# Performance work log

Hardware: AMD Instinct MI355X
Metric: run time of the kernel (lower is better)

The kernel has to match this reference:

```python
import jax, jax.numpy as jnp
import numpy as np

T = 2048            # flattened tokens (vLLM style)
D = 4096            # hidden_size
NSSM = 128          # ssm_state_size
K = 4               # conv kernel size
G = 8               # n_groups
H = 128             # mamba_num_heads
P = 64              # mamba_head_dim
INTER = H * P       # 8192 = expand * hidden_size
CONV_DIM = INTER + 2 * G * NSSM   # 10240 (x, B, C share the conv)
PROJ = INTER + CONV_DIM + H       # 18560 (z, xBC, dt)
Q = 128             # SSD chunk size
EPS = 1e-5


def setup_inputs() -> dict:
    key = jax.random.key(0)
    ks = jax.random.split(key, 9)
    s = 0.02
    return {
        "hidden_states": jax.random.normal(ks[0], (T, D), jnp.float32),
        "residual": jax.random.normal(ks[1], (T, D), jnp.float32),
        "norm_w": jnp.ones((D,), jnp.float32),
        "in_proj_w": jax.random.normal(ks[2], (PROJ, D), jnp.float32) * s,
        "conv_w": jax.random.normal(ks[3], (CONV_DIM, K), jnp.float32) * 0.2,
        "conv_b": jax.random.normal(ks[4], (CONV_DIM,), jnp.float32) * 0.1,
        "A_log": jnp.log(jax.random.uniform(ks[5], (H,), jnp.float32, 1.0, 16.0)),
        "D_res": jax.random.normal(ks[6], (H,), jnp.float32) * 0.5 + 1.0,
        "dt_bias": jax.random.normal(ks[7], (H,), jnp.float32) * 0.5,
        "gn_w": jnp.ones((INTER,), jnp.float32),
        "out_proj_w": jax.random.normal(ks[8], (D, INTER), jnp.float32) * s,
    }


def _forward(hidden_states, residual, norm_w, in_proj_w, conv_w, conv_b,
             A_log, D_res, dt_bias, gn_w, out_proj_w):
    # ---- fused add + RMSNorm (vLLM RMSNorm(hidden, residual)) ----
    resid = hidden_states + residual
    hs = resid * jax.lax.rsqrt(jnp.mean(resid * resid, -1, keepdims=True) + EPS) * norm_w

    # ---- MambaMixer2 ----
    proj = hs @ in_proj_w.T                              # [T, PROJ]
    z, xBC, dt = jnp.split(proj, [INTER, INTER + CONV_DIM], axis=-1)

    # causal depthwise conv1d over time + SiLU
    xp = jnp.pad(xBC, ((K - 1, 0), (0, 0)))
    conv = conv_b + sum(conv_w[:, k] * xp[k:k + T] for k in range(K))
    xBC = jax.nn.silu(conv)

    x, B, C = jnp.split(xBC, [INTER, INTER + G * NSSM], axis=-1)
    x = x.reshape(T, H, P)
    Bh = jnp.repeat(B.reshape(T, G, NSSM), H // G, axis=1)   # [T,H,N]
    Ch = jnp.repeat(C.reshape(T, G, NSSM), H // G, axis=1)   # [T,H,N]

    dt = jax.nn.softplus(dt + dt_bias)                   # [T,H]
    A = -jnp.exp(A_log)                                  # [H] (negative)

    # ---- SSD chunked selective scan ----
    NC = T // Q
    a = (dt * A).reshape(NC, Q, H)                       # per-step log decay (<=0)
    cum = jnp.cumsum(a, axis=1)                          # inclusive cumsum, [NC,Q,H]
    Xd = (dt[:, :, None] * x).reshape(NC, Q, H, P)
    Bc = Bh.reshape(NC, Q, H, NSSM)
    Cc = Ch.reshape(NC, Q, H, NSSM)

    # intra-chunk: Y[i] = sum_{j<=i} (C_i.B_j) exp(cum_i-cum_j) Xd_j
    CB = jnp.einsum('cqhn,ckhn->chqk', Cc, Bc)
    cumT = cum.transpose(0, 2, 1)                        # [NC,H,Q]
    mask = jnp.tril(jnp.ones((Q, Q), bool))
    Lm = jnp.where(mask, jnp.exp(cumT[:, :, :, None] - cumT[:, :, None, :]), 0.0)
    Y = jnp.einsum('chqk,ckhp->cqhp', CB * Lm, Xd)

    # chunk-local end states, then scan states across chunks
    cum_end = cum[:, -1]                                 # [NC,H]
    decay_out = jnp.exp(cum_end[:, None] - cum)          # [NC,Q,H]
    S_loc = jnp.einsum('cqhn,cqh,cqhp->chnp', Bc, decay_out, Xd)
    chunk_decay = jnp.exp(cum_end)                       # [NC,H]

    def step(s, inp):
        dec, sl = inp
        return dec[:, None, None] * s + sl, s            # emit state BEFORE chunk

    _, S_prev = jax.lax.scan(step, jnp.zeros((H, NSSM, P), x.dtype),
                             (chunk_decay, S_loc))       # [NC,H,N,P]

    # inter-chunk contribution + skip connection D*x
    Y = Y + jnp.einsum('cqhn,cqh,chnp->cqhp', Cc, jnp.exp(cum), S_prev)
    y = Y.reshape(T, H, P) + D_res[None, :, None] * x

    # gated RMSNorm then out projection
    y = y.reshape(T, INTER) * jax.nn.silu(z)
    y = y * jax.lax.rsqrt(jnp.mean(y * y, -1, keepdims=True) + EPS) * gn_w
    return y @ out_proj_w.T, resid


def reference(hidden_states, residual, norm_w, in_proj_w, conv_w, conv_b,
              A_log, D_res, dt_bias, gn_w, out_proj_w):
    return _forward(hidden_states, residual, norm_w, in_proj_w, conv_w, conv_b,
                    A_log, D_res, dt_bias, gn_w, out_proj_w)
```

## Files before the change

### kernel.cpp

```cpp
#include <hip/hip_runtime.h>
#include <stdint.h>

typedef unsigned short u16;
typedef unsigned int   u32;
typedef float  f32x4  __attribute__((ext_vector_type(4)));
typedef __bf16 bf16x8 __attribute__((ext_vector_type(8)));
typedef u16    u16x4  __attribute__((ext_vector_type(4)));
typedef u16    u16x8  __attribute__((ext_vector_type(8)));

#define T_N     2048
#define D_N     4096
#define H_N     128
#define P_N     64
#define G_N     8
#define NS_N    128
#define INTER_N 8192
#define CONVD_N 10240
#define PROJ_N  18560
#define NGEMM_N 18432
#define NC_N    16

__device__ __forceinline__ float bf2f(u16 u){ u32 x = ((u32)u) << 16; return __builtin_bit_cast(float, x); }
__device__ __forceinline__ u16 f2bf(float f){
  u32 u = __builtin_bit_cast(u32, f);
  u += 0x7FFFu + ((u >> 16) & 1u);
  return (u16)(u >> 16);
}

__device__ __forceinline__ void gld_lds16(const void* g, void* lds){
  __builtin_amdgcn_global_load_lds(
      (const __attribute__((address_space(1))) void*)(uintptr_t)g,
      (__attribute__((address_space(3))) void*)(u32)(uintptr_t)lds,
      16, 0, 0);
}

__global__ __launch_bounds__(256)
void k_addnorm(const float* __restrict__ hin, const float* __restrict__ rin,
               const float* __restrict__ nw, float* __restrict__ resid,
               u16* __restrict__ hs16, float* __restrict__ rstd){
  __shared__ float red[4];
  const int row = blockIdx.x, tid = threadIdx.x;
  const size_t rb = (size_t)row * D_N;
  f32x4 s[4];
  float ss = 0.f;
  #pragma unroll
  for (int i = 0; i < 4; ++i){
    int c4 = tid + i*256;
    f32x4 a = *(const f32x4*)&hin[rb + (size_t)c4*4];
    f32x4 b = *(const f32x4*)&rin[rb + (size_t)c4*4];
    s[i] = a + b;
    *(f32x4*)&resid[rb + (size_t)c4*4] = s[i];
    ss += s[i][0]*s[i][0] + s[i][1]*s[i][1] + s[i][2]*s[i][2] + s[i][3]*s[i][3];
  }
  #pragma unroll
  for (int o = 32; o > 0; o >>= 1) ss += __shfl_down(ss, o, 64);
  if ((tid & 63) == 0) red[tid >> 6] = ss;
  __syncthreads();
  float tot = (red[0] + red[1]) + (red[2] + red[3]);
  float rs = rsqrtf(tot / (float)D_N + 1e-5f);
  if (tid == 0) rstd[row] = rs;
  #pragma unroll
  for (int i = 0; i < 4; ++i){
    int c4 = tid + i*256;
    f32x4 w = *(const f32x4*)&nw[(size_t)c4*4];
    u16x4 o = { f2bf(s[i][0]*rs*w[0]), f2bf(s[i][1]*rs*w[1]),
                f2bf(s[i][2]*rs*w[2]), f2bf(s[i][3]*rs*w[3]) };
    *(u16x4*)&hs16[rb + (size_t)c4*4] = o;
  }
}

__global__ void k_cvt(const float* __restrict__ in, u16* __restrict__ out, size_t n4){
  size_t i = (size_t)blockIdx.x * blockDim.x + threadIdx.x;
  size_t stride = (size_t)gridDim.x * blockDim.x;
  for (; i < n4; i += stride){
    f32x4 v = *(const f32x4*)&in[i*4];
    u16x4 o = { f2bf(v[0]), f2bf(v[1]), f2bf(v[2]), f2bf(v[3]) };
    *(u16x4*)&out[i*4] = o;
  }
}

__global__ void k_wdt(const float* __restrict__ W, const float* __restrict__ nw,
                      float* __restrict__ Wn){
  int idx = blockIdx.x*256 + threadIdx.x;
  int d = idx >> 7, h = idx & 127;
  Wn[(size_t)d*128 + h] = W[(size_t)(INTER_N + CONVD_N + h)*D_N + d] * nw[d];
}

__global__ __launch_bounds__(256)
void k_dtgemm(const float* __restrict__ resid, const float* __restrict__ Wn,
              float* __restrict__ dtpart){
  __shared__ float lhs[16*128];
  const int tid = threadIdx.x;
  const int tb = blockIdx.x >> 3, ks = blockIdx.x & 7;
  const int t0 = tb * 16;
  const int k0 = ks * (D_N / 8);
  const int hcol = tid & 127, rh = tid >> 7;
  float acc[8] = {0,0,0,0,0,0,0,0};
  for (int kt = k0; kt < k0 + D_N/8; kt += 128){
    __syncthreads();
    #pragma unroll
    for (int it = 0; it < 2; ++it){
      int idx = it*256 + tid;
      int rr = idx >> 5, c4 = idx & 31;
      *(f32x4*)&lhs[rr*128 + c4*4] = *(const f32x4*)&resid[(size_t)(t0+rr)*D_N + kt + c4*4];
    }
    __syncthreads();
    #pragma unroll 4
    for (int kk4 = 0; kk4 < 32; ++kk4){
      f32x4 w4;
      #pragma unroll
      for (int j = 0; j < 4; ++j) w4[j] = Wn[(size_t)(kt + kk4*4 + j)*128 + hcol];
      #pragma unroll
      for (int j = 0; j < 8; ++j){
        f32x4 lv = *(const f32x4*)&lhs[(rh*8 + j)*128 + kk4*4];
        acc[j] += lv[0]*w4[0] + lv[1]*w4[1] + lv[2]*w4[2] + lv[3]*w4[3];
      }
    }
  }
  #pragma unroll
  for (int j = 0; j < 8; ++j){
    int t = t0 + rh*8 + j;
    dtpart[((size_t)ks*T_N + t)*128 + hcol] = acc[j];
  }
}

__global__ void k_dtprep(const float* __restrict__ dtpart, const float* __restrict__ rstd,
                         const float* __restrict__ dt_bias, const float* __restrict__ A_log,
                         float* __restrict__ dtv, float* __restrict__ cum,
                         float* __restrict__ cumend, float* __restrict__ dec){
  int c = blockIdx.x, h = threadIdx.x;
  float A = -expf(A_log[h]);
  float bias = dt_bias[h];
  float cm = 0.f;
  for (int q = 0; q < 128; ++q){
    int t = c*128 + q;
    float s = 0.f;
    #pragma unroll
    for (int kspl = 0; kspl < 8; ++kspl)
      s += dtpart[((size_t)kspl*T_N + t)*128 + h];
    float x = s * rstd[t] + bias;
    float dv = (x > 20.f) ? x : log1pf(expf(x));
    dtv[(size_t)t*128 + h] = dv;
    cm += dv * A;
    cum[(size_t)t*128 + h] = cm;
  }
  cumend[c*128 + h] = cm;
  dec[c*128 + h] = expf(cm);
}

#define STA(BUF,HH,KT) gld_lds16(pA + (size_t)((HH)*64)*K + (size_t)(KT)*64, shb + (BUF)*BSZ + (HH)*8192 + tid*16)
#define STB(BUF,HH,KT) gld_lds16(pB[HH] + (size_t)(KT)*64, shb + (BUF)*BSZ + 16384 + (HH)*8192 + tid*16)
#define VMWN do { asm volatile("s_waitcnt vmcnt(%0)" :: "n"(NFRAG) : "memory"); __builtin_amdgcn_sched_barrier(0); } while(0)
#define RDA(BUF, Q, V0, V1, V2, V3)                                                     \
    bf16x8 V0 = *(const bf16x8*)(shb + (BUF)*BSZ + rdA + (Q)*4096 + sA0);               \
    bf16x8 V1 = *(const bf16x8*)(shb + (BUF)*BSZ + rdA + (Q)*4096 + sA1);               \
    bf16x8 V2 = *(const bf16x8*)(shb + (BUF)*BSZ + rdA + (Q)*4096 + 2048 + sA0);        \
    bf16x8 V3 = *(const bf16x8*)(shb + (BUF)*BSZ + rdA + (Q)*4096 + 2048 + sA1);
#define RDB(BUF, BB)                                                                    \
    _Pragma("unroll") for (int nn = 0; nn < NFRAG; ++nn){                               \
      BB[nn][0] = *(const bf16x8*)(shb + (BUF)*BSZ + rdB + nn*2048 + sA0);              \
      BB[nn][1] = *(const bf16x8*)(shb + (BUF)*BSZ + rdB + nn*2048 + sA1);              \
    }
#define MM8(Q, V0, V1, V2, V3, BB)                                                      \
    _Pragma("unroll") for (int nn = 0; nn < NFRAG; ++nn){                               \
      acc[(Q)*2+0][nn] = __builtin_amdgcn_mfma_f32_16x16x32_bf16(V0, BB[nn][0], acc[(Q)*2+0][nn],0,0,0); \
      acc[(Q)*2+0][nn] = __builtin_amdgcn_mfma_f32_16x16x32_bf16(V1, BB[nn][1], acc[(Q)*2+0][nn],0,0,0); \
      acc[(Q)*2+1][nn] = __builtin_amdgcn_mfma_f32_16x16x32_bf16(V2, BB[nn][0], acc[(Q)*2+1][nn],0,0,0); \
      acc[(Q)*2+1][nn] = __builtin_amdgcn_mfma_f32_16x16x32_bf16(V3, BB[nn][1], acc[(Q)*2+1][nn],0,0,0); \
    }
#define ENDPH                                                                           \
    __builtin_amdgcn_s_setprio(0);                                                      \
    __builtin_amdgcn_s_barrier();                                                       \
    __builtin_amdgcn_sched_barrier(0);

template<int NFRAG, typename OT>
__global__ __launch_bounds__(512, 4)
void k_gemm256(const u16* __restrict__ A, const u16* __restrict__ Bm,
               OT* __restrict__ C, int ldc, int K, int nkt){
  constexpr int BSZ = 16384 + NFRAG*8192;
  __shared__ char shb[2*BSZ];
  const int tid = threadIdx.x, ln = tid & 63, wid = tid >> 6;
  const int wm = wid >> 2, wn = wid & 3;
  const int lr = ln & 15, lg = ln >> 4;

  const int gx = gridDim.x;
  const int mt = gridDim.y;
  const int lin = blockIdx.y * gx + blockIdx.x;
  const int xcd = lin & 7, sub = lin >> 3;
  const int ncx = gx >> 3;
  const int n_local = sub / mt;
  const int m_idx   = sub % mt;
  const int m0 = m_idx << 7;
  const int n0 = (xcd * ncx + n_local) * (NFRAG*64);

  const int srow = tid >> 3;
  const int slog = ((tid & 7) ^ (srow & 7)) * 8;
  const u16* pA = A + (size_t)(m0 + srow)*K + slog;
  const u16* pB[NFRAG];
  #pragma unroll
  for (int hh = 0; hh < NFRAG; ++hh)
    pB[hh] = Bm + (size_t)(n0 + hh*64 + srow)*K + slog;

  const int sA0 = (lg ^ (ln & 7)) << 4;
  const int sA1 = ((4 + lg) ^ (ln & 7)) << 4;
  const u32 rdA = wm*8192 + lr*128;
  const u32 rdB = 16384 + (wn*NFRAG*16 + lr)*128;

  f32x4 acc[4][NFRAG] = {};

  STA(0, 0, 0); STA(0, 1, 0);
  #pragma unroll
  for (int hh = 0; hh < NFRAG; ++hh) STB(0, hh, 0);
  #pragma unroll
  for (int hh = 0; hh < NFRAG; ++hh) STB(1, hh, 1);
  VMWN;
  __builtin_amdgcn_s_barrier();
  __builtin_amdgcn_sched_barrier(0);

  const int nit = nkt >> 1;
  #pragma unroll 1
  for (int it = 0; it < nit; ++it){
    const int t1 = 2*it + 1;
    int t2 = 2*it + 2; if (t2 >= nkt) t2 = 0;
    int t3 = 2*it + 3; if (t3 >= nkt) t3 = 1;
    bf16x8 bb0[NFRAG][2], bb1[NFRAG][2];
    {
      RDA(0,0, x0,x1,x2,x3) RDB(0, bb0)
      STA(1, 0, t1); STA(1, 1, t1);
      __builtin_amdgcn_s_setprio(1);
      MM8(0, x0,x1,x2,x3, bb0)
      ENDPH
    }
    {
      RDA(0,1, x0,x1,x2,x3)
      #pragma unroll
      for (int hh = 0; hh < NFRAG; ++hh) STB(0, hh, t2);
      VMWN;
      __builtin_amdgcn_s_setprio(1);
      MM8(1, x0,x1,x2,x3, bb0)
      ENDPH
    }
    {
      RDA(1,0, x0,x1,x2,x3) RDB(1, bb1)
      STA(0, 0, t2); STA(0, 1, t2);
      __builtin_amdgcn_s_setprio(1);
      MM8(0, x0,x1,x2,x3, bb1)
      ENDPH
    }
    {
      RDA(1,1, x0,x1,x2,x3)
      #pragma unroll
      for (int hh = 0; hh < NFRAG; ++hh) STB(1, hh, t3);
      VMWN;
      __builtin_amdgcn_s_setprio(1);
      MM8(1, x0,x1,x2,x3, bb1)
      ENDPH
    }
  }
  asm volatile("s_waitcnt vmcnt(0)" ::: "memory");

  const int crow = m0 + wm*64 + lg*4;
  const int ccol = n0 + wn*(NFRAG*16) + lr;
  #pragma unroll
  for (int m = 0; m < 4; ++m)
    #pragma unroll
    for (int nn = 0; nn < NFRAG; ++nn)
      #pragma unroll
      for (int r = 0; r < 4; ++r){
        float v = acc[m][nn][r];
        if constexpr (__is_same(OT, float))
          C[(size_t)(crow + m*16 + r)*ldc + ccol + nn*16] = v;
        else
          C[(size_t)(crow + m*16 + r)*ldc + ccol + nn*16] = f2bf(v);
      }
}

__global__ __launch_bounds__(256)
void k_conv(const u16* __restrict__ proj16, const float* __restrict__ cw,
            const float* __restrict__ cb, u16* __restrict__ x16,
            u16* __restrict__ B16, u16* __restrict__ C16){
  const int ch = blockIdx.x*256 + threadIdx.x;
  const int tbase = blockIdx.y*64;
  f32x4 w = *(const f32x4*)&cw[(size_t)ch*4];
  const float bias = cb[ch];
  const u16* pcol = proj16 + INTER_N + ch;
  float p0 = 0.f, p1 = 0.f, p2 = 0.f;
  if (tbase >= 3){
    p0 = bf2f(pcol[(size_t)(tbase-3)*PROJ_N]);
    p1 = bf2f(pcol[(size_t)(tbase-2)*PROJ_N]);
    p2 = bf2f(pcol[(size_t)(tbase-1)*PROJ_N]);
  }
  u16* xdst = (ch < INTER_N) ? x16 + ch
            : (ch < INTER_N + 1024) ? B16 + (ch - INTER_N)
            : C16 + (ch - INTER_N - 1024);
  const int dstride = (ch < INTER_N) ? INTER_N : 1024;
  #pragma unroll 4
  for (int i = 0; i < 64; ++i){
    int t = tbase + i;
    float cur = bf2f(pcol[(size_t)t*PROJ_N]);
    float acc = bias + w[0]*p0 + w[1]*p1 + w[2]*p2 + w[3]*cur;
    float v = acc / (1.f + __expf(-acc));
    xdst[(size_t)t*dstride] = f2bf(v);
    p0 = p1; p1 = p2; p2 = cur;
  }
}

__global__ __launch_bounds__(512)
void k_ssda(const u16* __restrict__ B16, const u16* __restrict__ x16,
            const float* __restrict__ dtv, const float* __restrict__ cum,
            const float* __restrict__ cumend, u16* __restrict__ SlocT){
  __shared__ u16 lBdT[128*136];
  __shared__ u16 lXdT[64*136];
  __shared__ float lDec[128], lDt[128];
  const int tid = threadIdx.x, wid = tid >> 6, ln = tid & 63;
  const int c = blockIdx.x >> 7, h = blockIdx.x & 127, g = h >> 4;
  if (tid < 128){
    int t = c*128 + tid;
    lDec[tid] = __expf(cumend[c*128 + h] - cum[(size_t)t*128 + h]);
    lDt[tid]  = dtv[(size_t)t*128 + h];
  }
  __syncthreads();
  for (int it = 0; it < 32; ++it){
    int idx = it*512 + tid;
    int q = idx >> 7, n = idx & 127;
    float bv = bf2f(B16[(size_t)(c*128 + q)*1024 + g*128 + n]) * lDec[q];
    lBdT[n*136 + q] = f2bf(bv);
  }
  for (int it = 0; it < 16; ++it){
    int idx = it*512 + tid;
    int q = idx >> 6, p = idx & 63;
    float xv = bf2f(x16[(size_t)(c*128 + q)*INTER_N + h*64 + p]) * lDt[q];
    lXdT[p*136 + q] = f2bf(xv);
  }
  __syncthreads();
  const int wr = wid >> 1, wc = wid & 1;
  const int kofs = (ln >> 4) << 3;
  f32x4 acc[2][2] = {};
  #pragma unroll
  for (int ks = 0; ks < 4; ++ks){
    bf16x8 a[2], b[2];
    #pragma unroll
    for (int m = 0; m < 2; ++m) a[m] = *(const bf16x8*)&lBdT[(wr*32 + m*16 + (ln & 15))*136 + ks*32 + kofs];
    #pragma unroll
    for (int n = 0; n < 2; ++n) b[n] = *(const bf16x8*)&lXdT[(wc*32 + n*16 + (ln & 15))*136 + ks*32 + kofs];
    #pragma unroll
    for (int m = 0; m < 2; ++m)
      #pragma unroll
      for (int n = 0; n < 2; ++n)
        acc[m][n] = __builtin_amdgcn_mfma_f32_16x16x32_bf16(a[m], b[n], acc[m][n], 0, 0, 0);
  }
  const size_t base = (size_t)(c*128 + h) * 8192;
  #pragma unroll
  for (int m = 0; m < 2; ++m)
    #pragma unroll
    for (int n = 0; n < 2; ++n){
      int p  = wc*32 + n*16 + (ln & 15);
      int nn = wr*32 + m*16 + ((ln >> 4) << 2);
      u16x4 o = { f2bf(acc[m][n][0]), f2bf(acc[m][n][1]), f2bf(acc[m][n][2]), f2bf(acc[m][n][3]) };
      *(u16x4*)&SlocT[base + (size_t)p*128 + nn] = o;
    }
}

__global__ __launch_bounds__(256)
void k_scan(const u16* __restrict__ SlocT, const float* __restrict__ dec,
            u16* __restrict__ SprevT){
  int idx = blockIdx.x*256 + threadIdx.x;
  int h = idx >> 11, p = (idx >> 5) & 63, n4 = idx & 31;
  float s0 = 0.f, s1 = 0.f, s2 = 0.f, s3 = 0.f;
  for (int c = 0; c < NC_N; ++c){
    size_t off = (size_t)(c*128 + h)*8192 + (size_t)p*128 + n4*4;
    u16x4 o = { f2bf(s0), f2bf(s1), f2bf(s2), f2bf(s3) };
    *(u16x4*)&SprevT[off] = o;
    u16x4 sl = *(const u16x4*)&SlocT[off];
    float d = dec[c*128 + h];
    s0 = d*s0 + bf2f(sl[0]); s1 = d*s1 + bf2f(sl[1]);
    s2 = d*s2 + bf2f(sl[2]); s3 = d*s3 + bf2f(sl[3]);
  }
}

__global__ __launch_bounds__(512)
void k_ssdb(const u16* __restrict__ C16, const u16* __restrict__ B16g,
            const u16* __restrict__ x16, const float* __restrict__ dtv,
            const float* __restrict__ cum, const u16* __restrict__ SprevT,
            const u16* __restrict__ proj16, const float* __restrict__ Dres,
            u16* __restrict__ yg16){
  __shared__ u16 lC[128*136];
  __shared__ u16 lBP[128*136];
  __shared__ u16 lXdT[64*136];
  __shared__ float lCum[128], lDt[128];
  const int tid = threadIdx.x, wid = tid >> 6, ln = tid & 63;
  const int c = blockIdx.x >> 7, h = blockIdx.x & 127, g = h >> 4;
  if (tid < 128){
    int t = c*128 + tid;
    lCum[tid] = cum[(size_t)t*128 + h];
    lDt[tid]  = dtv[(size_t)t*128 + h];
  }
  __syncthreads();
  for (int it = 0; it < 32; ++it){
    int idx = it*512 + tid;
    int q = idx >> 7, n = idx & 127;
    size_t gi = (size_t)(c*128 + q)*1024 + g*128 + n;
    lC[q*136 + n]  = C16[gi];
    lBP[q*136 + n] = B16g[gi];
  }
  for (int it = 0; it < 16; ++it){
    int idx = it*512 + tid;
    int q = idx >> 6, p = idx & 63;
    lXdT[p*136 + q] = f2bf(bf2f(x16[(size_t)(c*128 + q)*INTER_N + h*64 + p]) * lDt[q]);
  }
  __syncthreads();
  const int kofs = (ln >> 4) << 3;
  {
    const int wr = wid >> 2, wc = wid & 3;
    f32x4 cb[4][2] = {};
    #pragma unroll
    for (int ks = 0; ks < 4; ++ks){
      bf16x8 a[4], b[2];
      #pragma unroll
      for (int m = 0; m < 4; ++m) a[m] = *(const bf16x8*)&lC[(wr*64 + m*16 + (ln & 15))*136 + ks*32 + kofs];
      #pragma unroll
      for (int n = 0; n < 2; ++n) b[n] = *(const bf16x8*)&lBP[(wc*32 + n*16 + (ln & 15))*136 + ks*32 + kofs];
      #pragma unroll
      for (int m = 0; m < 4; ++m)
        #pragma unroll
        for (int n = 0; n < 2; ++n)
          cb[m][n] = __builtin_amdgcn_mfma_f32_16x16x32_bf16(a[m], b[n], cb[m][n], 0, 0, 0);
    }
    __syncthreads();
    #pragma unroll
    for (int m = 0; m < 4; ++m)
      #pragma unroll
      for (int n = 0; n < 2; ++n){
        int kcol = (wid & 3)*32 + n*16 + (ln & 15);
        float ck = lCum[kcol];
        #pragma unroll
        for (int r = 0; r < 4; ++r){
          int q = (wid >> 2)*64 + m*16 + ((ln >> 4) << 2) + r;
          float v = (kcol <= q) ? cb[m][n][r] * __expf(lCum[q] - ck) : 0.f;
          lBP[q*136 + kcol] = f2bf(v);
        }
      }
  }
  __syncthreads();
  const int yr = wid >> 1, yc = wid & 1;
  f32x4 y1[2][2] = {}, y2[2][2] = {};
  const size_t spbase = (size_t)(c*128 + h) * 8192;
  #pragma unroll
  for (int ks = 0; ks < 4; ++ks){
    bf16x8 ap[2], acf[2], bx[2], bs[2];
    #pragma unroll
    for (int m = 0; m < 2; ++m){
      int qr = yr*32 + m*16 + (ln & 15);
      ap[m]  = *(const bf16x8*)&lBP[qr*136 + ks*32 + kofs];
      acf[m] = *(const bf16x8*)&lC [qr*136 + ks*32 + kofs];
    }
    #pragma unroll
    for (int n = 0; n < 2; ++n){
      int p = yc*32 + n*16 + (ln & 15);
      bx[n] = *(const bf16x8*)&lXdT[p*136 + ks*32 + kofs];
      bs[n] = *(const bf16x8*)&SprevT[spbase + (size_t)p*128 + ks*32 + kofs];
    }
    #pragma unroll
    for (int m = 0; m < 2; ++m)
      #pragma unroll
      for (int n = 0; n < 2; ++n){
        y1[m][n] = __builtin_amdgcn_mfma_f32_16x16x32_bf16(ap[m],  bx[n], y1[m][n], 0, 0, 0);
        y2[m][n] = __builtin_amdgcn_mfma_f32_16x16x32_bf16(acf[m], bs[n], y2[m][n], 0, 0, 0);
      }
  }
  const float dh = Dres[h];
  #pragma unroll
  for (int m = 0; m < 2; ++m)
    #pragma unroll
    for (int r = 0; r < 4; ++r){
      int q = yr*32 + m*16 + ((ln >> 4) << 2) + r;
      float eq = __expf(lCum[q]);
      size_t t = (size_t)(c*128 + q);
      #pragma unroll
      for (int n = 0; n < 2; ++n){
        int p = yc*32 + n*16 + (ln & 15);
        int chn = h*64 + p;
        float xv = bf2f(x16[t*INTER_N + chn]);
        float zv = bf2f(proj16[t*PROJ_N + chn]);
        float yv = y1[m][n][r] + eq*y2[m][n][r] + dh*xv;
        float sg = zv / (1.f + __expf(-zv));
        yg16[t*INTER_N + chn] = f2bf(yv * sg);
      }
    }
}

__global__ __launch_bounds__(256)
void k_gnorm(const u16* __restrict__ yg, const float* __restrict__ gnw,
             u16* __restrict__ yn16){
  __shared__ float red[4];
  const int row = blockIdx.x, tid = threadIdx.x;
  const u16* rp = yg + (size_t)row * INTER_N;
  u16x8 v[4];
  float ss = 0.f;
  #pragma unroll
  for (int i = 0; i < 4; ++i){
    v[i] = *(const u16x8*)&rp[(size_t)(tid + i*256)*8];
    #pragma unroll
    for (int j = 0; j < 8; ++j){ float f = bf2f(v[i][j]); ss += f*f; }
  }
  #pragma unroll
  for (int o = 32; o > 0; o >>= 1) ss += __shfl_down(ss, o, 64);
  if ((tid & 63) == 0) red[tid >> 6] = ss;
  __syncthreads();
  float tot = (red[0] + red[1]) + (red[2] + red[3]);
  float sc = rsqrtf(tot / (float)INTER_N + 1e-5f);
  #pragma unroll
  for (int i = 0; i < 4; ++i){
    int c8 = (tid + i*256)*8;
    u16x8 o;
    #pragma unroll
    for (int j = 0; j < 8; ++j)
      o[j] = f2bf(bf2f(v[i][j]) * sc * gnw[c8 + j]);
    *(u16x8*)&yn16[(size_t)row*INTER_N + c8] = o;
  }
}

extern "C" void kernel_launch(void* const* d_in, const int* in_sizes, int n_in,
                              void* d_out, int out_size, void* d_ws, size_t ws_size,
                              hipStream_t stream){
  (void)in_sizes; (void)n_in; (void)out_size;
  const float* hs_in     = (const float*)d_in[0];
  const float* res_in    = (const float*)d_in[1];
  const float* norm_w    = (const float*)d_in[2];
  const float* in_proj_w = (const float*)d_in[3];
  const float* conv_w    = (const float*)d_in[4];
  const float* conv_b    = (const float*)d_in[5];
  const float* A_log     = (const float*)d_in[6];
  const float* D_res     = (const float*)d_in[7];
  const float* dt_bias   = (const float*)d_in[8];
  const float* gn_w      = (const float*)d_in[9];
  const float* out_proj_w= (const float*)d_in[10];

  float* out0      = (float*)d_out;
  float* resid_out = out0 + (size_t)T_N * D_N;

  char* ws = (char*)d_ws;
  const size_t o_hs16   = 0;
  const size_t o_Win16  = 16777216;
  const size_t o_Wout16 = 168820736;
  const size_t o_proj   = 235929600;
  const size_t o_Wn     = 387973120;
  const size_t o_dtv    = 391118848;
  const size_t o_cum    = 392167424;
  const size_t o_cumend = 393216000;
  const size_t o_dec    = 393224192;
  const size_t o_rstd   = 393232384;
  const size_t o_x16    = 393240576;
  const size_t o_B16    = 426795008;
  const size_t o_C16    = 430989312;
  const size_t o_SlocT  = 435183616;
  const size_t o_SprevT = 468738048;
  const size_t o_yn16   = 502292480;
  const size_t WS_NEED  = 535846912;
  if (ws_size < WS_NEED) return;

  u16*   hs16   = (u16*)  (ws + o_hs16);
  u16*   Win16  = (u16*)  (ws + o_Win16);
  u16*   Wout16 = (u16*)  (ws + o_Wout16);
  u16*   proj16 = (u16*)  (ws + o_proj);
  float* Wn     = (float*)(ws + o_Wn);
  float* dtpart = (float*)(ws + o_proj);
  float* dtv    = (float*)(ws + o_dtv);
  float* cum    = (float*)(ws + o_cum);
  float* cumend = (float*)(ws + o_cumend);
  float* dec    = (float*)(ws + o_dec);
  float* rstd   = (float*)(ws + o_rstd);
  u16*   x16    = (u16*)  (ws + o_x16);
  u16*   B16    = (u16*)  (ws + o_B16);
  u16*   C16    = (u16*)  (ws + o_C16);
  u16*   SlocT  = (u16*)  (ws + o_SlocT);
  u16*   SprevT = (u16*)  (ws + o_SprevT);
  u16*   yn16   = (u16*)  (ws + o_yn16);
  u16*   yg16   = (u16*)  (ws + o_Win16);

  k_addnorm<<<T_N, 256, 0, stream>>>(hs_in, res_in, norm_w, resid_out, hs16, rstd);
  k_cvt<<<4096, 256, 0, stream>>>(in_proj_w,  Win16,  (size_t)NGEMM_N * D_N / 4);
  k_cvt<<<2048, 256, 0, stream>>>(out_proj_w, Wout16, (size_t)D_N * INTER_N / 4);
  k_wdt<<<2048, 256, 0, stream>>>(in_proj_w, norm_w, Wn);
  k_dtgemm<<<1024, 256, 0, stream>>>(resid_out, Wn, dtpart);
  k_dtprep<<<NC_N, 128, 0, stream>>>(dtpart, rstd, dt_bias, A_log, dtv, cum, cumend, dec);
  k_gemm256<3, u16><<<dim3(NGEMM_N/192, T_N/128), 512, 0, stream>>>(hs16, Win16, proj16, PROJ_N, D_N, D_N/64);
  k_conv<<<dim3(CONVD_N/256, T_N/64), 256, 0, stream>>>(proj16, conv_w, conv_b, x16, B16, C16);
  k_ssda<<<NC_N * H_N, 512, 0, stream>>>(B16, x16, dtv, cum, cumend, SlocT);
  k_scan<<<1024, 256, 0, stream>>>(SlocT, dec, SprevT);
  k_ssdb<<<NC_N * H_N, 512, 0, stream>>>(C16, B16, x16, dtv, cum, SprevT, proj16, D_res, yg16);
  k_gnorm<<<T_N, 256, 0, stream>>>(yg16, gn_w, yn16);
  k_gemm256<2, float><<<dim3(D_N/128, T_N/128), 512, 0, stream>>>(yn16, Wout16, out0, D_N, INTER_N, INTER_N/64);
}
```

Baseline: 931.3 us.

## Rework GEMM kernel to 4 waves with larger per-wave tiles

The two main GEMMs move from a 512-thread, 8-wave block to a 256-thread, 4-wave block (2x2 wave grid). Each wave now computes a 64 x NF*16 tile (96 or 64 columns), which raises MFMA work per LDS fragment read and improves register-level reuse. Global-to-LDS staging is reorganized into 32-row slices with a single B pointer, and occupancy is lowered to 2 blocks per CU. The trade-off is higher register pressure and fewer waves available to hide latency.

```diff
diff --git a/kernel.cpp b/kernel.cpp
--- a/kernel.cpp
+++ b/kernel.cpp
@@ -148,39 +148,39 @@
   dec[c*128 + h] = expf(cm);
 }
 
-#define STA(BUF,HH,KT) gld_lds16(pA + (size_t)((HH)*64)*K + (size_t)(KT)*64, shb + (BUF)*BSZ + (HH)*8192 + tid*16)
-#define STB(BUF,HH,KT) gld_lds16(pB[HH] + (size_t)(KT)*64, shb + (BUF)*BSZ + 16384 + (HH)*8192 + tid*16)
-#define VMWN do { asm volatile("s_waitcnt vmcnt(%0)" :: "n"(NFRAG) : "memory"); __builtin_amdgcn_sched_barrier(0); } while(0)
-#define RDA(BUF, Q, V0, V1, V2, V3)                                                     \
-    bf16x8 V0 = *(const bf16x8*)(shb + (BUF)*BSZ + rdA + (Q)*4096 + sA0);               \
-    bf16x8 V1 = *(const bf16x8*)(shb + (BUF)*BSZ + rdA + (Q)*4096 + sA1);               \
-    bf16x8 V2 = *(const bf16x8*)(shb + (BUF)*BSZ + rdA + (Q)*4096 + 2048 + sA0);        \
-    bf16x8 V3 = *(const bf16x8*)(shb + (BUF)*BSZ + rdA + (Q)*4096 + 2048 + sA1);
-#define RDB(BUF, BB)                                                                    \
-    _Pragma("unroll") for (int nn = 0; nn < NFRAG; ++nn){                               \
+#define STA(BUF,HH,KT) gld_lds16(pA + (size_t)((HH)*32)*K + (size_t)(KT)*64, shb + (BUF)*BSZ + (HH)*4096 + tid*16)
+#define STB(BUF,HH,KT) gld_lds16(pB + (size_t)((HH)*32)*K + (size_t)(KT)*64, shb + (BUF)*BSZ + 16384 + (HH)*4096 + tid*16)
+#define VMWN do { asm volatile("s_waitcnt vmcnt(%0)" :: "n"(NF) : "memory"); __builtin_amdgcn_sched_barrier(0); } while(0)
+#define RDA4(BUF, MOFF)                                                                 \
+    bf16x8 a0 = *(const bf16x8*)(shb + (BUF)*BSZ + rdA + (MOFF)*2048 + sA0);            \
+    bf16x8 a1 = *(const bf16x8*)(shb + (BUF)*BSZ + rdA + (MOFF)*2048 + sA1);            \
+    bf16x8 a2 = *(const bf16x8*)(shb + (BUF)*BSZ + rdA + ((MOFF)+1)*2048 + sA0);        \
+    bf16x8 a3 = *(const bf16x8*)(shb + (BUF)*BSZ + rdA + ((MOFF)+1)*2048 + sA1);
+#define RDBALL(BUF, BB)                                                                 \
+    _Pragma("unroll") for (int nn = 0; nn < NF; ++nn){                                  \
       BB[nn][0] = *(const bf16x8*)(shb + (BUF)*BSZ + rdB + nn*2048 + sA0);              \
       BB[nn][1] = *(const bf16x8*)(shb + (BUF)*BSZ + rdB + nn*2048 + sA1);              \
     }
-#define MM8(Q, V0, V1, V2, V3, BB)                                                      \
-    _Pragma("unroll") for (int nn = 0; nn < NFRAG; ++nn){                               \
-      acc[(Q)*2+0][nn] = __builtin_amdgcn_mfma_f32_16x16x32_bf16(V0, BB[nn][0], acc[(Q)*2+0][nn],0,0,0); \
-      acc[(Q)*2+0][nn] = __builtin_amdgcn_mfma_f32_16x16x32_bf16(V1, BB[nn][1], acc[(Q)*2+0][nn],0,0,0); \
-      acc[(Q)*2+1][nn] = __builtin_amdgcn_mfma_f32_16x16x32_bf16(V2, BB[nn][0], acc[(Q)*2+1][nn],0,0,0); \
-      acc[(Q)*2+1][nn] = __builtin_amdgcn_mfma_f32_16x16x32_bf16(V3, BB[nn][1], acc[(Q)*2+1][nn],0,0,0); \
+#define MM24(MOFF, BB)                                                                  \
+    _Pragma("unroll") for (int nn = 0; nn < NF; ++nn){                                  \
+      acc[(MOFF)+0][nn] = __builtin_amdgcn_mfma_f32_16x16x32_bf16(a0, BB[nn][0], acc[(MOFF)+0][nn],0,0,0); \
+      acc[(MOFF)+0][nn] = __builtin_amdgcn_mfma_f32_16x16x32_bf16(a1, BB[nn][1], acc[(MOFF)+0][nn],0,0,0); \
+      acc[(MOFF)+1][nn] = __builtin_amdgcn_mfma_f32_16x16x32_bf16(a2, BB[nn][0], acc[(MOFF)+1][nn],0,0,0); \
+      acc[(MOFF)+1][nn] = __builtin_amdgcn_mfma_f32_16x16x32_bf16(a3, BB[nn][1], acc[(MOFF)+1][nn],0,0,0); \
     }
 #define ENDPH                                                                           \
     __builtin_amdgcn_s_setprio(0);                                                      \
     __builtin_amdgcn_s_barrier();                                                       \
     __builtin_amdgcn_sched_barrier(0);
 
-template<int NFRAG, typename OT>
-__global__ __launch_bounds__(512, 4)
-void k_gemm256(const u16* __restrict__ A, const u16* __restrict__ Bm,
-               OT* __restrict__ C, int ldc, int K, int nkt){
-  constexpr int BSZ = 16384 + NFRAG*8192;
+template<int NF, typename OT>
+__global__ __launch_bounds__(256, 2)
+void k_gemmw(const u16* __restrict__ A, const u16* __restrict__ Bm,
+             OT* __restrict__ C, int ldc, int K, int nkt){
+  constexpr int BSZ = 16384 + NF*4096;
   __shared__ char shb[2*BSZ];
   const int tid = threadIdx.x, ln = tid & 63, wid = tid >> 6;
-  const int wm = wid >> 2, wn = wid & 3;
+  const int wm = wid >> 1, wn = wid & 1;
   const int lr = ln & 15, lg = ln >> 4;
 
   const int gx = gridDim.x;
@@ -191,28 +191,25 @@
   const int n_local = sub / mt;
   const int m_idx   = sub % mt;
   const int m0 = m_idx << 7;
-  const int n0 = (xcd * ncx + n_local) * (NFRAG*64);
+  const int n0 = (xcd * ncx + n_local) * (NF*32);
 
   const int srow = tid >> 3;
   const int slog = ((tid & 7) ^ (srow & 7)) * 8;
   const u16* pA = A + (size_t)(m0 + srow)*K + slog;
-  const u16* pB[NFRAG];
-  #pragma unroll
-  for (int hh = 0; hh < NFRAG; ++hh)
-    pB[hh] = Bm + (size_t)(n0 + hh*64 + srow)*K + slog;
+  const u16* pB = Bm + (size_t)(n0 + srow)*K + slog;
 
   const int sA0 = (lg ^ (ln & 7)) << 4;
   const int sA1 = ((4 + lg) ^ (ln & 7)) << 4;
   const u32 rdA = wm*8192 + lr*128;
-  const u32 rdB = 16384 + (wn*NFRAG*16 + lr)*128;
-
-  f32x4 acc[4][NFRAG] = {};
-
-  STA(0, 0, 0); STA(0, 1, 0);
-  #pragma unroll
-  for (int hh = 0; hh < NFRAG; ++hh) STB(0, hh, 0);
-  #pragma unroll
-  for (int hh = 0; hh < NFRAG; ++hh) STB(1, hh, 1);
+  const u32 rdB = 16384 + wn*(NF*2048) + lr*128;
+
+  f32x4 acc[4][NF] = {};
+
+  STA(0,0,0); STA(0,1,0); STA(0,2,0); STA(0,3,0);
+  #pragma unroll
+  for (int hh = 0; hh < NF; ++hh) STB(0, hh, 0);
+  #pragma unroll
+  for (int hh = 0; hh < NF; ++hh) STB(1, hh, 1);
   VMWN;
   __builtin_amdgcn_s_barrier();
   __builtin_amdgcn_sched_barrier(0);
@@ -223,48 +220,48 @@
     const int t1 = 2*it + 1;
     int t2 = 2*it + 2; if (t2 >= nkt) t2 = 0;
     int t3 = 2*it + 3; if (t3 >= nkt) t3 = 1;
-    bf16x8 bb0[NFRAG][2], bb1[NFRAG][2];
+    bf16x8 bb0[NF][2], bb1[NF][2];
     {
-      RDA(0,0, x0,x1,x2,x3) RDB(0, bb0)
-      STA(1, 0, t1); STA(1, 1, t1);
+      RDA4(0, 0) RDBALL(0, bb0)
+      STA(1,0,t1); STA(1,1,t1); STA(1,2,t1); STA(1,3,t1);
       __builtin_amdgcn_s_setprio(1);
-      MM8(0, x0,x1,x2,x3, bb0)
+      MM24(0, bb0)
       ENDPH
     }
     {
-      RDA(0,1, x0,x1,x2,x3)
-      #pragma unroll
-      for (int hh = 0; hh < NFRAG; ++hh) STB(0, hh, t2);
+      RDA4(0, 2)
+      #pragma unroll
+      for (int hh = 0; hh < NF; ++hh) STB(0, hh, t2);
       VMWN;
       __builtin_amdgcn_s_setprio(1);
-      MM8(1, x0,x1,x2,x3, bb0)
+      MM24(2, bb0)
       ENDPH
     }
     {
-      RDA(1,0, x0,x1,x2,x3) RDB(1, bb1)
-      STA(0, 0, t2); STA(0, 1, t2);
+      RDA4(1, 0) RDBALL(1, bb1)
+      STA(0,0,t2); STA(0,1,t2); STA(0,2,t2); STA(0,3,t2);
       __builtin_amdgcn_s_setprio(1);
-      MM8(0, x0,x1,x2,x3, bb1)
+      MM24(0, bb1)
       ENDPH
     }
     {
-      RDA(1,1, x0,x1,x2,x3)
-      #pragma unroll
-      for (int hh = 0; hh < NFRAG; ++hh) STB(1, hh, t3);
+      RDA4(1, 2)
+      #pragma unroll
+      for (int hh = 0; hh < NF; ++hh) STB(1, hh, t3);
       VMWN;
       __builtin_amdgcn_s_setprio(1);
-      MM8(1, x0,x1,x2,x3, bb1)
+      MM24(2, bb1)
       ENDPH
     }
   }
   asm volatile("s_waitcnt vmcnt(0)" ::: "memory");
 
   const int crow = m0 + wm*64 + lg*4;
-  const int ccol = n0 + wn*(NFRAG*16) + lr;
+  const int ccol = n0 + wn*(NF*16) + lr;
   #pragma unroll
   for (int m = 0; m < 4; ++m)
     #pragma unroll
-    for (int nn = 0; nn < NFRAG; ++nn)
+    for (int nn = 0; nn < NF; ++nn)
       #pragma unroll
       for (int r = 0; r < 4; ++r){
         float v = acc[m][nn][r];
@@ -584,11 +581,11 @@
   k_wdt<<<2048, 256, 0, stream>>>(in_proj_w, norm_w, Wn);
   k_dtgemm<<<1024, 256, 0, stream>>>(resid_out, Wn, dtpart);
   k_dtprep<<<NC_N, 128, 0, stream>>>(dtpart, rstd, dt_bias, A_log, dtv, cum, cumend, dec);
-  k_gemm256<3, u16><<<dim3(NGEMM_N/192, T_N/128), 512, 0, stream>>>(hs16, Win16, proj16, PROJ_N, D_N, D_N/64);
+  k_gemmw<6, u16><<<dim3(NGEMM_N/192, T_N/128), 256, 0, stream>>>(hs16, Win16, proj16, PROJ_N, D_N, D_N/64);
   k_conv<<<dim3(CONVD_N/256, T_N/64), 256, 0, stream>>>(proj16, conv_w, conv_b, x16, B16, C16);
   k_ssda<<<NC_N * H_N, 512, 0, stream>>>(B16, x16, dtv, cum, cumend, SlocT);
   k_scan<<<1024, 256, 0, stream>>>(SlocT, dec, SprevT);
   k_ssdb<<<NC_N * H_N, 512, 0, stream>>>(C16, B16, x16, dtv, cum, SprevT, proj16, D_res, yg16);
   k_gnorm<<<T_N, 256, 0, stream>>>(yg16, gn_w, yn16);
-  k_gemm256<2, float><<<dim3(D_N/128, T_N/128), 512, 0, stream>>>(yn16, Wout16, out0, D_N, INTER_N, INTER_N/64);
-}
+  k_gemmw<4, float><<<dim3(D_N/128, T_N/128), 256, 0, stream>>>(yn16, Wout16, out0, D_N, INTER_N, INTER_N/64);
+}
```

Result: no change. 921.7 us (-1.0%).
